# Optimization experiments

Hardware: AMD Instinct MI355X
Metric: run time of the kernel (lower is better)

Reference implementation:

```python
import jax, jax.numpy as jnp
import numpy as np

T = 8192
N_EMBD = 1024
HEAD_SIZE = 64
NEG_FILL = -1e9


def setup_inputs() -> dict:
    key = jax.random.key(0)
    kq, kk, kv, kwq, kwk, kwv = jax.random.split(key, 6)
    s = 1.0 / np.sqrt(N_EMBD)
    return {
        "encodings_for_q": jax.random.normal(kq, (T, N_EMBD), dtype=jnp.float32),
        "encodings_for_k": jax.random.normal(kk, (T, N_EMBD), dtype=jnp.float32),
        "encodings_for_v": jax.random.normal(kv, (T, N_EMBD), dtype=jnp.float32),
        # causal mask: True above the diagonal -> positions to mask out
        "mask": jnp.triu(jnp.ones((T, T), dtype=bool), k=1),
        # torch Linear weights have shape [out_features, in_features]
        "W_q": jax.random.normal(kwq, (HEAD_SIZE, N_EMBD), dtype=jnp.float32) * s,
        "W_k": jax.random.normal(kwk, (HEAD_SIZE, N_EMBD), dtype=jnp.float32) * s,
        "W_v": jax.random.normal(kwv, (HEAD_SIZE, N_EMBD), dtype=jnp.float32) * s,
    }


def reference(encodings_for_q, encodings_for_k, encodings_for_v, mask, W_q, W_k, W_v):
    # projections: x @ W.T  (torch nn.Linear, bias=False)
    q = jnp.einsum("te,he->th", encodings_for_q, W_q)  # [T, H]
    k = jnp.einsum("te,he->th", encodings_for_k, W_k)  # [T, H]
    v = jnp.einsum("te,he->th", encodings_for_v, W_v)  # [T, H]
    scale = 1.0 / jnp.sqrt(jnp.asarray(HEAD_SIZE, dtype=q.dtype))
    sims = jnp.einsum("th,sh->ts", q, k) * scale       # [T, T]
    sims = jnp.where(mask, jnp.asarray(NEG_FILL, dtype=sims.dtype), sims)
    attn = jax.nn.softmax(sims, axis=1)                # softmax over col_dim=1
    return jnp.einsum("ts,sh->th", attn, v)            # [T, H]
```

## Files before the change

kernel.cpp:

```cpp
#include <hip/hip_runtime.h>
#include <hip/hip_bf16.h>
#include <stdint.h>

#define T_DIM 8192
#define E_DIM 1024
#define H_DIM 64
#define NEGF  -3.0e38f

typedef __attribute__((ext_vector_type(8))) short bf16x8;
typedef __attribute__((ext_vector_type(4))) float f32x4;

static __device__ __forceinline__ uint32_t pk2(float x, float y) {
    __hip_bfloat162 h = __float22bfloat162_rn(make_float2(x, y));
    union { __hip_bfloat162 h2; uint32_t u; } c; c.h2 = h; return c.u;
}
static __device__ __forceinline__ bf16x8 pack8(float4 a, float4 b) {
    union { bf16x8 v; uint32_t u[4]; } c;
    c.u[0] = pk2(a.x, a.y); c.u[1] = pk2(a.z, a.w);
    c.u[2] = pk2(b.x, b.y); c.u[3] = pk2(b.z, b.w);
    return c.v;
}
static __device__ __forceinline__ uint16_t bf1(float x) {
    __hip_bfloat16 h = __float2bfloat16(x);
    union { __hip_bfloat16 h1; uint16_t s; } c; c.h1 = h; return c.s;
}

__global__ __launch_bounds__(256) void wconv_kernel(
    const float* __restrict__ Wq, const float* __restrict__ Wk, const float* __restrict__ Wv,
    uint16_t* __restrict__ Wqb, uint16_t* __restrict__ Wkb, uint16_t* __restrict__ Wvb)
{
    const int idx = blockIdx.x * 256 + threadIdx.x;
    const int which = idx / 16384;
    const int off = (idx & 16383) * 4;
    const float* W = (which == 0) ? Wq : (which == 1) ? Wk : Wv;
    uint16_t* Wb   = (which == 0) ? Wqb : (which == 1) ? Wkb : Wvb;
    float4 w = *(const float4*)(W + off);
    uint2 o = make_uint2(pk2(w.x, w.y), pk2(w.z, w.w));
    *(uint2*)(Wb + off) = o;
}

__global__ __launch_bounds__(256) void proj_kernel(
    const float* __restrict__ Xq, const float* __restrict__ Xk, const float* __restrict__ Xv,
    const uint16_t* __restrict__ Wqb, const uint16_t* __restrict__ Wkb, const uint16_t* __restrict__ Wvb,
    uint16_t* __restrict__ Qb, uint16_t* __restrict__ Kb, uint16_t* __restrict__ Vtb)
{
    __shared__ float TD[64][69];

    const int mat = blockIdx.y;
    const float* X    = (mat == 0) ? Xq  : (mat == 1) ? Xk  : Xv;
    const uint16_t* W = (mat == 0) ? Wqb : (mat == 1) ? Wkb : Wvb;

    const int tid  = threadIdx.x;
    const int wv   = tid >> 6;
    const int lane = tid & 63;
    const int lidx = lane & 15;
    const int quad = lane >> 4;
    const int t0   = blockIdx.x * 64 + wv * 16;

    const float* Xr = X + (size_t)(t0 + lidx) * E_DIM + quad * 8;

    f32x4 acc[4] = {{0,0,0,0},{0,0,0,0},{0,0,0,0},{0,0,0,0}};
    for (int k0 = 0; k0 < E_DIM; k0 += 32) {
        float4 x0 = *(const float4*)(Xr + k0);
        float4 x1 = *(const float4*)(Xr + k0 + 4);
        bf16x8 xa = pack8(x0, x1);
        #pragma unroll
        for (int nt = 0; nt < 4; ++nt) {
            const uint16_t* Wr = W + (size_t)(nt * 16 + lidx) * E_DIM + k0 + quad * 8;
            bf16x8 wb = *(const bf16x8*)Wr;
            acc[nt] = __builtin_amdgcn_mfma_f32_16x16x32_bf16(xa, wb, acc[nt], 0, 0, 0);
        }
    }

    if (mat < 2) {
        uint16_t* O = (mat == 0) ? Qb : Kb;
        #pragma unroll
        for (int nt = 0; nt < 4; ++nt)
            #pragma unroll
            for (int r = 0; r < 4; ++r)
                O[(size_t)(t0 + quad * 4 + r) * H_DIM + nt * 16 + lidx] = bf1(acc[nt][r]);
    } else {
        #pragma unroll
        for (int nt = 0; nt < 4; ++nt)
            #pragma unroll
            for (int r = 0; r < 4; ++r)
                TD[wv * 16 + quad * 4 + r][nt * 16 + lidx] = acc[nt][r];
        __syncthreads();
        const int h = tid >> 2, tq = tid & 3;
        uint32_t w8[8];
        #pragma unroll
        for (int i = 0; i < 8; ++i)
            w8[i] = pk2(TD[tq * 16 + 2 * i][h], TD[tq * 16 + 2 * i + 1][h]);
        uint16_t* dst = Vtb + (size_t)h * T_DIM + blockIdx.x * 64 + tq * 16;
        uint4 lo = make_uint4(w8[0], w8[1], w8[2], w8[3]);
        uint4 hi = make_uint4(w8[4], w8[5], w8[6], w8[7]);
        *(uint4*)dst       = lo;
        *(uint4*)(dst + 8) = hi;
    }
}

__global__ __launch_bounds__(256) void flash_kernel(
    const uint16_t* __restrict__ Qb, const uint16_t* __restrict__ Kb,
    const uint16_t* __restrict__ Vtb, float* __restrict__ Out)
{
    __shared__ __align__(16) float WS[4][16][68];
    __shared__ float Mw[4][16];
    __shared__ float Lw[4][16];

    const int tid  = threadIdx.x;
    const int wv   = tid >> 6;
    const int lane = tid & 63;
    const int lidx = lane & 15;
    const int quad = lane >> 4;

    const int qt = 511 - (int)blockIdx.x;
    const int q0 = qt * 16;

    bf16x8 aq0 = *(const bf16x8*)(Qb + (size_t)(q0 + lidx) * H_DIM + quad * 8);
    bf16x8 aq1 = *(const bf16x8*)(Qb + (size_t)(q0 + lidx) * H_DIM + 32 + quad * 8);

    const int ktiles  = qt / 4 + 1;
    const int base    = ktiles >> 2;
    const int rem     = ktiles & 3;
    const int myn     = base + (wv < rem ? 1 : 0);
    const int mystart = wv * base + (wv < rem ? wv : rem);

    float m[4] = {NEGF, NEGF, NEGF, NEGF};
    float l[4] = {0.f, 0.f, 0.f, 0.f};
    f32x4 o[4] = {{0,0,0,0},{0,0,0,0},{0,0,0,0},{0,0,0,0}};

    for (int it = 0; it < myn; ++it) {
        const int kt = mystart + it;
        const int s0 = kt * 64;

        f32x4 s[4];
        #pragma unroll
        for (int nt = 0; nt < 4; ++nt) {
            const uint16_t* kr = Kb + (size_t)(s0 + nt * 16 + lidx) * H_DIM + quad * 8;
            bf16x8 b0 = *(const bf16x8*)(kr);
            bf16x8 b1 = *(const bf16x8*)(kr + 32);
            f32x4 z = {0, 0, 0, 0};
            s[nt] = __builtin_amdgcn_mfma_f32_16x16x32_bf16(aq0, b0, z, 0, 0, 0);
            s[nt] = __builtin_amdgcn_mfma_f32_16x16x32_bf16(aq1, b1, s[nt], 0, 0, 0);
        }

        if (kt == ktiles - 1) {
            #pragma unroll
            for (int nt = 0; nt < 4; ++nt)
                #pragma unroll
                for (int r = 0; r < 4; ++r) {
                    const int col = s0 + nt * 16 + lidx;
                    const int row = q0 + quad * 4 + r;
                    s[nt][r] = (col <= row) ? s[nt][r] * 0.125f : NEGF;
                }
        } else {
            #pragma unroll
            for (int nt = 0; nt < 4; ++nt)
                #pragma unroll
                for (int r = 0; r < 4; ++r)
                    s[nt][r] *= 0.125f;
        }

        #pragma unroll
        for (int r = 0; r < 4; ++r) {
            float mt = fmaxf(fmaxf(s[0][r], s[1][r]), fmaxf(s[2][r], s[3][r]));
            mt = fmaxf(mt, __shfl_xor(mt, 1));
            mt = fmaxf(mt, __shfl_xor(mt, 2));
            mt = fmaxf(mt, __shfl_xor(mt, 4));
            mt = fmaxf(mt, __shfl_xor(mt, 8));
            const float mn = fmaxf(m[r], mt);
            const float al = __expf(m[r] - mn);
            m[r] = mn;
            float ps = 0.f;
            #pragma unroll
            for (int nt = 0; nt < 4; ++nt) {
                const float pv = __expf(s[nt][r] - mn);
                WS[wv][quad * 4 + r][nt * 16 + lidx] = pv;
                ps += pv;
            }
            ps += __shfl_xor(ps, 1);
            ps += __shfl_xor(ps, 2);
            ps += __shfl_xor(ps, 4);
            ps += __shfl_xor(ps, 8);
            l[r] = l[r] * al + ps;
            #pragma unroll
            for (int nt = 0; nt < 4; ++nt) o[nt][r] *= al;
        }

        const float* pr = &WS[wv][lidx][0];
        float4 p0 = *(const float4*)(pr + quad * 8);
        float4 p1 = *(const float4*)(pr + quad * 8 + 4);
        float4 p2 = *(const float4*)(pr + 32 + quad * 8);
        float4 p3 = *(const float4*)(pr + 32 + quad * 8 + 4);
        bf16x8 ap0 = pack8(p0, p1);
        bf16x8 ap1 = pack8(p2, p3);

        #pragma unroll
        for (int nt = 0; nt < 4; ++nt) {
            const uint16_t* vr = Vtb + (size_t)(nt * 16 + lidx) * T_DIM + s0 + quad * 8;
            bf16x8 v0 = *(const bf16x8*)(vr);
            bf16x8 v1 = *(const bf16x8*)(vr + 32);
            o[nt] = __builtin_amdgcn_mfma_f32_16x16x32_bf16(ap0, v0, o[nt], 0, 0, 0);
            o[nt] = __builtin_amdgcn_mfma_f32_16x16x32_bf16(ap1, v1, o[nt], 0, 0, 0);
        }
    }

    if (lidx == 0) {
        #pragma unroll
        for (int r = 0; r < 4; ++r) { Mw[wv][quad * 4 + r] = m[r]; Lw[wv][quad * 4 + r] = l[r]; }
    }
    #pragma unroll
    for (int nt = 0; nt < 4; ++nt)
        #pragma unroll
        for (int r = 0; r < 4; ++r)
            WS[wv][quad * 4 + r][nt * 16 + lidx] = o[nt][r];
    __syncthreads();

    const int row = tid >> 4, cg = tid & 15;
    float M = fmaxf(fmaxf(Mw[0][row], Mw[1][row]), fmaxf(Mw[2][row], Mw[3][row]));
    float L = 0.f;
    float ox = 0.f, oy = 0.f, oz = 0.f, ow = 0.f;
    #pragma unroll
    for (int w2 = 0; w2 < 4; ++w2) {
        const float sc = __expf(Mw[w2][row] - M);
        L += Lw[w2][row] * sc;
        float4 t = *(const float4*)&WS[w2][row][cg * 4];
        ox += t.x * sc; oy += t.y * sc; oz += t.z * sc; ow += t.w * sc;
    }
    const float inv = 1.f / L;
    float4 ov = make_float4(ox * inv, oy * inv, oz * inv, ow * inv);
    *(float4*)(Out + (size_t)(q0 + row) * H_DIM + cg * 4) = ov;
}

extern "C" void kernel_launch(void* const* d_in, const int* in_sizes, int n_in,
                              void* d_out, int out_size, void* d_ws, size_t ws_size,
                              hipStream_t stream) {
    (void)in_sizes; (void)n_in; (void)out_size; (void)ws_size;
    const float* Xq = (const float*)d_in[0];
    const float* Xk = (const float*)d_in[1];
    const float* Xv = (const float*)d_in[2];
    const float* Wq = (const float*)d_in[4];
    const float* Wk = (const float*)d_in[5];
    const float* Wv = (const float*)d_in[6];

    uint16_t* Qb  = (uint16_t*)d_ws;
    uint16_t* Kb  = Qb + (size_t)T_DIM * H_DIM;
    uint16_t* Vtb = Kb + (size_t)T_DIM * H_DIM;
    uint16_t* Wqb = Vtb + (size_t)T_DIM * H_DIM;
    uint16_t* Wkb = Wqb + (size_t)H_DIM * E_DIM;
    uint16_t* Wvb = Wkb + (size_t)H_DIM * E_DIM;

    wconv_kernel<<<192, 256, 0, stream>>>(Wq, Wk, Wv, Wqb, Wkb, Wvb);

    dim3 pgrid(T_DIM / 64, 3);
    proj_kernel<<<pgrid, 256, 0, stream>>>(Xq, Xk, Xv, Wqb, Wkb, Wvb, Qb, Kb, Vtb);

    flash_kernel<<<T_DIM / 16, 256, 0, stream>>>(Qb, Kb, Vtb, (float*)d_out);
}
```

Measured before the change: 490.7 us.

## Compute transposed S tile so P stays in registers, use exp2 softmax

Result: slower. 521.2 us (+6.2%).

```diff
diff --git a/kernel.cpp b/kernel.cpp
--- a/kernel.cpp
+++ b/kernel.cpp
@@ -6,9 +6,12 @@
 #define E_DIM 1024
 #define H_DIM 64
 #define NEGF  -3.0e38f
+#define SC_LOG2 0.18033688011112042f
 
 typedef __attribute__((ext_vector_type(8))) short bf16x8;
 typedef __attribute__((ext_vector_type(4))) float f32x4;
+
+static __device__ __forceinline__ float fexp2(float x) { return __builtin_amdgcn_exp2f(x); }
 
 static __device__ __forceinline__ uint32_t pk2(float x, float y) {
     __hip_bfloat162 h = __float22bfloat162_rn(make_float2(x, y));
@@ -19,6 +22,11 @@
     c.u[0] = pk2(a.x, a.y); c.u[1] = pk2(a.z, a.w);
     c.u[2] = pk2(b.x, b.y); c.u[3] = pk2(b.z, b.w);
     return c.v;
+}
+static __device__ __forceinline__ bf16x8 mk8(uint32_t a, uint32_t b, uint32_t c, uint32_t d) {
+    union { bf16x8 v; uint32_t u[4]; } t;
+    t.u[0] = a; t.u[1] = b; t.u[2] = c; t.u[3] = d;
+    return t.v;
 }
 static __device__ __forceinline__ uint16_t bf1(float x) {
     __hip_bfloat16 h = __float2bfloat16(x);
@@ -115,9 +123,10 @@
 
     const int qt = 511 - (int)blockIdx.x;
     const int q0 = qt * 16;
-
-    bf16x8 aq0 = *(const bf16x8*)(Qb + (size_t)(q0 + lidx) * H_DIM + quad * 8);
-    bf16x8 aq1 = *(const bf16x8*)(Qb + (size_t)(q0 + lidx) * H_DIM + 32 + quad * 8);
+    const int qg = q0 + lidx;
+
+    bf16x8 bq0 = *(const bf16x8*)(Qb + (size_t)qg * H_DIM + quad * 8);
+    bf16x8 bq1 = *(const bf16x8*)(Qb + (size_t)qg * H_DIM + 32 + quad * 8);
 
     const int ktiles  = qt / 4 + 1;
     const int base    = ktiles >> 2;
@@ -125,8 +134,7 @@
     const int myn     = base + (wv < rem ? 1 : 0);
     const int mystart = wv * base + (wv < rem ? wv : rem);
 
-    float m[4] = {NEGF, NEGF, NEGF, NEGF};
-    float l[4] = {0.f, 0.f, 0.f, 0.f};
+    float m = NEGF, l = 0.f;
     f32x4 o[4] = {{0,0,0,0},{0,0,0,0},{0,0,0,0},{0,0,0,0}};
 
     for (int it = 0; it < myn; ++it) {
@@ -137,11 +145,11 @@
         #pragma unroll
         for (int nt = 0; nt < 4; ++nt) {
             const uint16_t* kr = Kb + (size_t)(s0 + nt * 16 + lidx) * H_DIM + quad * 8;
-            bf16x8 b0 = *(const bf16x8*)(kr);
-            bf16x8 b1 = *(const bf16x8*)(kr + 32);
+            bf16x8 a0 = *(const bf16x8*)(kr);
+            bf16x8 a1 = *(const bf16x8*)(kr + 32);
             f32x4 z = {0, 0, 0, 0};
-            s[nt] = __builtin_amdgcn_mfma_f32_16x16x32_bf16(aq0, b0, z, 0, 0, 0);
-            s[nt] = __builtin_amdgcn_mfma_f32_16x16x32_bf16(aq1, b1, s[nt], 0, 0, 0);
+            s[nt] = __builtin_amdgcn_mfma_f32_16x16x32_bf16(a0, bq0, z, 0, 0, 0);
+            s[nt] = __builtin_amdgcn_mfma_f32_16x16x32_bf16(a1, bq1, s[nt], 0, 0, 0);
         }
 
         if (kt == ktiles - 1) {
@@ -149,71 +157,76 @@
             for (int nt = 0; nt < 4; ++nt)
                 #pragma unroll
                 for (int r = 0; r < 4; ++r) {
-                    const int col = s0 + nt * 16 + lidx;
-                    const int row = q0 + quad * 4 + r;
-                    s[nt][r] = (col <= row) ? s[nt][r] * 0.125f : NEGF;
+                    const int key = s0 + nt * 16 + quad * 4 + r;
+                    s[nt][r] = (key <= qg) ? s[nt][r] * SC_LOG2 : NEGF;
                 }
         } else {
             #pragma unroll
             for (int nt = 0; nt < 4; ++nt)
                 #pragma unroll
                 for (int r = 0; r < 4; ++r)
-                    s[nt][r] *= 0.125f;
-        }
-
-        #pragma unroll
-        for (int r = 0; r < 4; ++r) {
-            float mt = fmaxf(fmaxf(s[0][r], s[1][r]), fmaxf(s[2][r], s[3][r]));
-            mt = fmaxf(mt, __shfl_xor(mt, 1));
-            mt = fmaxf(mt, __shfl_xor(mt, 2));
-            mt = fmaxf(mt, __shfl_xor(mt, 4));
-            mt = fmaxf(mt, __shfl_xor(mt, 8));
-            const float mn = fmaxf(m[r], mt);
-            const float al = __expf(m[r] - mn);
-            m[r] = mn;
-            float ps = 0.f;
-            #pragma unroll
-            for (int nt = 0; nt < 4; ++nt) {
-                const float pv = __expf(s[nt][r] - mn);
-                WS[wv][quad * 4 + r][nt * 16 + lidx] = pv;
-                ps += pv;
+                    s[nt][r] *= SC_LOG2;
+        }
+
+        float mt = NEGF;
+        #pragma unroll
+        for (int nt = 0; nt < 4; ++nt)
+            #pragma unroll
+            for (int r = 0; r < 4; ++r)
+                mt = fmaxf(mt, s[nt][r]);
+        mt = fmaxf(mt, __shfl_xor(mt, 16));
+        mt = fmaxf(mt, __shfl_xor(mt, 32));
+        const float mn = fmaxf(fmaxf(m, mt), -1.0e30f);
+        const float alpha = fexp2(m - mn);
+        m = mn;
+
+        float p[4][4];
+        float ps = 0.f;
+        #pragma unroll
+        for (int nt = 0; nt < 4; ++nt)
+            #pragma unroll
+            for (int r = 0; r < 4; ++r) {
+                p[nt][r] = fexp2(s[nt][r] - mn);
+                ps += p[nt][r];
             }
-            ps += __shfl_xor(ps, 1);
-            ps += __shfl_xor(ps, 2);
-            ps += __shfl_xor(ps, 4);
-            ps += __shfl_xor(ps, 8);
-            l[r] = l[r] * al + ps;
-            #pragma unroll
-            for (int nt = 0; nt < 4; ++nt) o[nt][r] *= al;
-        }
-
-        const float* pr = &WS[wv][lidx][0];
-        float4 p0 = *(const float4*)(pr + quad * 8);
-        float4 p1 = *(const float4*)(pr + quad * 8 + 4);
-        float4 p2 = *(const float4*)(pr + 32 + quad * 8);
-        float4 p3 = *(const float4*)(pr + 32 + quad * 8 + 4);
-        bf16x8 ap0 = pack8(p0, p1);
-        bf16x8 ap1 = pack8(p2, p3);
-
-        #pragma unroll
-        for (int nt = 0; nt < 4; ++nt) {
-            const uint16_t* vr = Vtb + (size_t)(nt * 16 + lidx) * T_DIM + s0 + quad * 8;
-            bf16x8 v0 = *(const bf16x8*)(vr);
-            bf16x8 v1 = *(const bf16x8*)(vr + 32);
-            o[nt] = __builtin_amdgcn_mfma_f32_16x16x32_bf16(ap0, v0, o[nt], 0, 0, 0);
-            o[nt] = __builtin_amdgcn_mfma_f32_16x16x32_bf16(ap1, v1, o[nt], 0, 0, 0);
-        }
-    }
-
-    if (lidx == 0) {
-        #pragma unroll
-        for (int r = 0; r < 4; ++r) { Mw[wv][quad * 4 + r] = m[r]; Lw[wv][quad * 4 + r] = l[r]; }
-    }
+        ps += __shfl_xor(ps, 16);
+        ps += __shfl_xor(ps, 32);
+        l = l * alpha + ps;
+
+        float av[4];
+        #pragma unroll
+        for (int r = 0; r < 4; ++r) av[r] = __shfl(alpha, quad * 4 + r);
+        #pragma unroll
+        for (int ht = 0; ht < 4; ++ht)
+            #pragma unroll
+            for (int r = 0; r < 4; ++r)
+                o[ht][r] *= av[r];
+
+        bf16x8 ap0 = pack8(make_float4(p[0][0], p[0][1], p[0][2], p[0][3]),
+                           make_float4(p[1][0], p[1][1], p[1][2], p[1][3]));
+        bf16x8 ap1 = pack8(make_float4(p[2][0], p[2][1], p[2][2], p[2][3]),
+                           make_float4(p[3][0], p[3][1], p[3][2], p[3][3]));
+
+        #pragma unroll
+        for (int t = 0; t < 2; ++t) {
+            const bf16x8 ap = t ? ap1 : ap0;
+            #pragma unroll
+            for (int ht = 0; ht < 4; ++ht) {
+                const uint16_t* vr = Vtb + (size_t)(ht * 16 + lidx) * T_DIM + s0 + 32 * t + quad * 4;
+                uint2 va = *(const uint2*)(vr);
+                uint2 vb = *(const uint2*)(vr + 16);
+                bf16x8 bv = mk8(va.x, va.y, vb.x, vb.y);
+                o[ht] = __builtin_amdgcn_mfma_f32_16x16x32_bf16(ap, bv, o[ht], 0, 0, 0);
+            }
+        }
+    }
+
+    if (quad == 0) { Mw[wv][lidx] = m; Lw[wv][lidx] = l; }
     #pragma unroll
-    for (int nt = 0; nt < 4; ++nt)
+    for (int ht = 0; ht < 4; ++ht)
         #pragma unroll
         for (int r = 0; r < 4; ++r)
-            WS[wv][quad * 4 + r][nt * 16 + lidx] = o[nt][r];
+            WS[wv][quad * 4 + r][ht * 16 + lidx] = o[ht][r];
     __syncthreads();
 
     const int row = tid >> 4, cg = tid & 15;
@@ -222,7 +235,7 @@
     float ox = 0.f, oy = 0.f, oz = 0.f, ow = 0.f;
     #pragma unroll
     for (int w2 = 0; w2 < 4; ++w2) {
-        const float sc = __expf(Mw[w2][row] - M);
+        const float sc = fexp2(Mw[w2][row] - M);
         L += Lw[w2][row] * sc;
         float4 t = *(const float4*)&WS[w2][row][cg * 4];
         ox += t.x * sc; oy += t.y * sc; oz += t.z * sc; ow += t.w * sc;
```
